# Kernel tuning notes

Measured on AMD Instinct MI355X. Metric: run time of the kernel, lower is better.

Reference implementation:

```python
import jax, jax.numpy as jnp
import numpy as np

VOCAB, EMB, QLEN, DLEN, K = 100000, 300, 256, 8192, 5


def prelu(x, a):
    return jnp.where(x >= 0, x, a * x)


def apply_conv(x, filt, a):
    # x: (L, E), filt: (E, 1, fs, E) -- matches torch F.conv2d(OIHW)
    fs = filt.shape[2]
    pad = fs // 2 + 1
    inp = x[None, None, :, :]  # (1,1,L,E)
    out = jax.lax.conv_general_dilated(
        inp, filt, window_strides=(1, 1), padding=[(pad, pad), (0, 0)],
        dimension_numbers=('NCHW', 'OIHW', 'NCHW'))  # (1,E,L',1)
    out = prelu(out, a)
    out = out[:, :, -x.shape[0]:, 0]          # keep last L rows -> (1,E,L)
    out = jnp.transpose(out, (0, 2, 1))[0]    # (L,E)
    return out + x


def cosine_sim(A, B):
    # (Q,E) x (D,E) -> (Q,D)
    num = A @ B.T
    den = jnp.linalg.norm(A, axis=1)[:, None] * jnp.linalg.norm(B, axis=1)[None, :]
    return num / den


def pool(sim):
    # sort-based k-max pooling == top_k (same set of values)
    top = jax.lax.top_k(sim, K)[0]           # (Q,K) descending
    avg = top.sum(-1) / float(K)
    mx = top[..., 0]
    return jnp.stack([mx, avg], axis=-1)      # (Q,2)


def score(pooled_list, w1, b1, w2, b2, a1, a2):
    x = jnp.concatenate(pooled_list, axis=-1)  # (Q,8)
    lo = prelu(x @ w1.T + b1, a1)              # dropout is identity in eval
    lo = prelu(lo @ w2.T + b2, a2)[..., 0]     # (Q,)
    return lo.sum(-1) / lo.shape[-1]


def setup_inputs() -> dict:
    key = jax.random.key(0)
    ks = jax.random.split(key, 12)
    doc1 = jax.random.randint(ks[0], (DLEN,), 0, VOCAB)
    doc2 = jax.random.randint(ks[1], (DLEN,), 0, VOCAB)
    question = jax.random.randint(ks[2], (QLEN,), 0, VOCAB)
    doc1_sim = jax.random.uniform(ks[3], (DLEN, QLEN), dtype=jnp.float32)
    doc2_sim = jax.random.uniform(ks[4], (DLEN, QLEN), dtype=jnp.float32)
    embeds = jax.random.normal(ks[5], (VOCAB, EMB), dtype=jnp.float32)
    filt_bi = jax.random.normal(ks[6], (EMB, 1, 2, EMB), dtype=jnp.float32)
    filt_tri = jax.random.normal(ks[7], (EMB, 1, 3, EMB), dtype=jnp.float32)
    w1 = jax.random.normal(ks[8], (8, 8), dtype=jnp.float32) * 0.3
    b1 = jnp.zeros((8,), jnp.float32)
    w2 = jax.random.normal(ks[9], (1, 8), dtype=jnp.float32) * 0.3
    b2 = jnp.zeros((1,), jnp.float32)
    a_bi = jnp.float32(0.25); a_tri = jnp.float32(0.25)
    a1 = jnp.float32(0.25); a2 = jnp.float32(0.25)
    return dict(doc1=doc1, doc2=doc2, question=question, doc1_sim=doc1_sim,
                doc2_sim=doc2_sim, embeds=embeds, filt_bi=filt_bi,
                filt_tri=filt_tri, a_bi=a_bi, a_tri=a_tri, w1=w1, b1=b1,
                w2=w2, b2=b2, a1=a1, a2=a2)


def reference(doc1, doc2, question, doc1_sim, doc2_sim, embeds, filt_bi,
              filt_tri, a_bi, a_tri, w1, b1, w2, b2, a1, a2):
    sim_oh1 = doc1_sim.T  # (Q,D)
    sim_oh2 = doc2_sim.T
    qe = embeds[question]
    d1e = embeds[doc1]
    d2e = embeds[doc2]
    qmask = (question > 1).astype(jnp.float32)
    m1 = qmask[:, None] * (doc1 > 1).astype(jnp.float32)[None, :]
    m2 = qmask[:, None] * (doc2 > 1).astype(jnp.float32)[None, :]
    ins1 = cosine_sim(qe, d1e) * m1
    ins2 = cosine_sim(qe, d2e) * m2
    q_bi = apply_conv(qe, filt_bi, a_bi)
    q_tri = apply_conv(qe, filt_tri, a_tri)
    d1_bi = apply_conv(d1e, filt_bi, a_bi)
    d1_tri = apply_conv(d1e, filt_tri, a_tri)
    d2_bi = apply_conv(d2e, filt_bi, a_bi)
    d2_tri = apply_conv(d2e, filt_tri, a_tri)
    s1_bi = cosine_sim(q_bi, d1_bi)
    s2_bi = cosine_sim(q_bi, d2_bi)
    s1_tri = cosine_sim(q_tri, d1_tri)
    s2_tri = cosine_sim(q_tri, d2_tri)
    d1_emit = score([pool(sim_oh1), pool(ins1), pool(s1_bi), pool(s1_tri)],
                    w1, b1, w2, b2, a1, a2)
    d2_emit = score([pool(sim_oh2), pool(ins2), pool(s2_bi), pool(s2_tri)],
                    w1, b1, w2, b2, a1, a2)
    # MarginRankingLoss(margin=0.9), y=1, batch of 1
    loss1 = jnp.maximum(0.0, -(d1_emit - d2_emit) + 0.9)
    loss2 = loss1 * 0.0
    return (loss1, d1_emit, d2_emit, loss1, loss2)
```

## Files before the change

### kernel.cpp

```cpp
#include <hip/hip_runtime.h>

#define EMB   300
#define QLEN  256
#define DLEN  8192
#define KTOP  5
#define STR   320
#define STRB  640

typedef __attribute__((ext_vector_type(8))) short short8v;
typedef __attribute__((ext_vector_type(4))) float f32x4;

__device__ inline float bf2f(short u) {
    return __uint_as_float(((unsigned int)(unsigned short)u) << 16);
}
__device__ inline short f2bf(float f) {
    unsigned int x = __float_as_uint(f);
    unsigned int r = x + 0x7fffu + ((x >> 16) & 1u);
    return (short)(r >> 16);
}
__device__ inline void gload_lds16(const void* g, void* l) {
    __builtin_amdgcn_global_load_lds((const __attribute__((address_space(1))) void*)g,
                                     (__attribute__((address_space(3))) void*)l, 16, 0, 0);
}
__device__ inline int swz128(int a) { return a ^ (((a >> 7) & 7) << 4); }

#define INSERT5(arr, v)                                                          \
    if ((v) > arr[4]) {                                                          \
        arr[4] = (v);                                                            \
        if (arr[4] > arr[3]) { float t_ = arr[4]; arr[4] = arr[3]; arr[3] = t_; }\
        if (arr[3] > arr[2]) { float t_ = arr[3]; arr[3] = arr[2]; arr[2] = t_; }\
        if (arr[2] > arr[1]) { float t_ = arr[2]; arr[2] = arr[1]; arr[1] = t_; }\
        if (arr[1] > arr[0]) { float t_ = arr[1]; arr[1] = arr[0]; arr[0] = t_; }\
    }

struct PrepArgs {
    const float* embeds;
    const int* toks[3]; short* out[3]; float* ssq[3]; int rows[3];
    const float* filt[2]; short* fout[2];
};

__global__ void prep(PrepArgs pa) {
    int W = blockIdx.x * 4 + (threadIdx.x >> 6);
    int lane = threadIdx.x & 63;
    int e0 = lane * 8;
    if (W < 16664) {
        int s, r;
        if (W < 264) { s = 0; r = W; }
        else if (W < 8464) { s = 1; r = W - 264; }
        else { s = 2; r = W - 8464; }
        int rows = pa.rows[s];
        short8v ov = {0, 0, 0, 0, 0, 0, 0, 0};
        float sum = 0.f;
        if (r < rows && e0 < 300) {
            const float* src = pa.embeds + (long)pa.toks[s][r] * EMB;
            float4 f0 = *(const float4*)(src + e0);
            ov[0] = f2bf(f0.x); ov[1] = f2bf(f0.y); ov[2] = f2bf(f0.z); ov[3] = f2bf(f0.w);
            sum = f0.x * f0.x + f0.y * f0.y + f0.z * f0.z + f0.w * f0.w;
            if (e0 < 296) {
                float4 f1 = *(const float4*)(src + e0 + 4);
                ov[4] = f2bf(f1.x); ov[5] = f2bf(f1.y); ov[6] = f2bf(f1.z); ov[7] = f2bf(f1.w);
                sum += f1.x * f1.x + f1.y * f1.y + f1.z * f1.z + f1.w * f1.w;
            }
        }
        if (e0 < STR) *(short8v*)(pa.out[s] + (long)r * STR + e0) = ov;
        #pragma unroll
        for (int off = 32; off > 0; off >>= 1) sum += __shfl_down(sum, off, 64);
        if (lane == 0 && r < rows) pa.ssq[s][r] = sum;
    } else {
        int w2 = W - 16664;
        int s = (w2 < 768) ? 0 : 1;
        int R = (s == 0) ? w2 : w2 - 768;
        int o = (s == 0) ? (R >> 1) : (R / 3);
        short8v ov = {0, 0, 0, 0, 0, 0, 0, 0};
        if (o < EMB && e0 < 300) {
            const float* src = pa.filt[s] + (long)R * EMB;
            float4 f0 = *(const float4*)(src + e0);
            ov[0] = f2bf(f0.x); ov[1] = f2bf(f0.y); ov[2] = f2bf(f0.z); ov[3] = f2bf(f0.w);
            if (e0 < 296) {
                float4 f1 = *(const float4*)(src + e0 + 4);
                ov[4] = f2bf(f1.x); ov[5] = f2bf(f1.y); ov[6] = f2bf(f1.z); ov[7] = f2bf(f1.w);
            }
        }
        if (e0 < STR) *(short8v*)(pa.fout[s] + (long)R * STR + e0) = ov;
    }
}

#define GEMM_PRELUDE64                                                        \
    int tid = threadIdx.x, lane = tid & 63, w = tid >> 6;                     \
    int wr = w >> 1, wc = w & 1;                                              \
    int arow[2], acol[2], brow[4], bcol[4];                                   \
    _Pragma("unroll")                                                         \
    for (int i_ = 0; i_ < 2; ++i_) {                                          \
        int lg_ = swz128(w * 2048 + i_ * 1024 + lane * 16);                   \
        arow[i_] = lg_ >> 7; acol[i_] = lg_ & 127;                            \
    }                                                                         \
    _Pragma("unroll")                                                         \
    for (int i_ = 0; i_ < 4; ++i_) {                                          \
        int lg_ = swz128(w * 4096 + i_ * 1024 + lane * 16);                   \
        brow[i_] = lg_ >> 7; bcol[i_] = lg_ & 127;                            \
    }

#define STAGE64(t) do { int kb_ = (t) * 128;                                  \
    _Pragma("unroll")                                                         \
    for (int i_ = 0; i_ < 2; ++i_)                                            \
        gload_lds16(Ab + (size_t)arow[i_] * STRB + kb_ + acol[i_],            \
                    AsB + w * 2048 + i_ * 1024);                              \
    _Pragma("unroll")                                                         \
    for (int i_ = 0; i_ < 4; ++i_)                                            \
        gload_lds16(Bb + (size_t)brow[i_] * ldbB + kb_ + bcol[i_],            \
                    BsB + w * 4096 + i_ * 1024);                              \
    } while (0)

#define COMPUTE64 do {                                                        \
    _Pragma("unroll")                                                         \
    for (int h_ = 0; h_ < 2; ++h_) {                                          \
        short8v a_[2], b_[4];                                                 \
        _Pragma("unroll")                                                     \
        for (int f_ = 0; f_ < 2; ++f_) {                                      \
            int la_ = (wr * 32 + f_ * 16 + (lane & 15)) * 128                 \
                      + ((lane >> 4) << 4) + h_ * 64;                         \
            a_[f_] = *(const short8v*)(AsB + swz128(la_));                    \
        }                                                                     \
        _Pragma("unroll")                                                     \
        for (int f_ = 0; f_ < 4; ++f_) {                                      \
            int lb_ = (wc * 64 + f_ * 16 + (lane & 15)) * 128                 \
                      + ((lane >> 4) << 4) + h_ * 64;                         \
            b_[f_] = *(const short8v*)(BsB + swz128(lb_));                    \
        }                                                                     \
        _Pragma("unroll")                                                     \
        for (int mf_ = 0; mf_ < 2; ++mf_)                                     \
            _Pragma("unroll")                                                 \
            for (int nf_ = 0; nf_ < 4; ++nf_)                                 \
                acc[mf_][nf_] = __builtin_amdgcn_mfma_f32_16x16x32_bf16(      \
                    a_[mf_], b_[nf_], acc[mf_][nf_], 0, 0, 0);                \
    } } while (0)

#define GEMM_MAIN64(nt) do {                                                  \
    for (int t_ = 0; t_ < (nt); ++t_) {                                       \
        if (t_ > 0) __syncthreads();                                          \
        STAGE64(t_);                                                          \
        __syncthreads();                                                      \
        COMPUTE64;                                                            \
    } } while (0)

__device__ inline void topk_reduce_store(float top[KTOP], float (*buf)[KTOP], int t,
                                         float* feat, int q, int c0) {
    #pragma unroll
    for (int i = 0; i < KTOP; ++i) buf[t][i] = top[i];
    __syncthreads();
    for (int stride = 128; stride >= 1; stride >>= 1) {
        if (t < stride) {
            float arr[KTOP];
            #pragma unroll
            for (int i = 0; i < KTOP; ++i) arr[i] = buf[t][i];
            #pragma unroll
            for (int r = 0; r < KTOP; ++r) { float v = buf[t + stride][r]; INSERT5(arr, v); }
            #pragma unroll
            for (int i = 0; i < KTOP; ++i) buf[t][i] = arr[i];
        }
        __syncthreads();
    }
    if (t == 0) {
        float mx = buf[0][0];
        float sum = buf[0][0] + buf[0][1] + buf[0][2] + buf[0][3] + buf[0][4];
        feat[(long)q * 8 + c0] = mx;
        feat[(long)q * 8 + c0 + 1] = sum / (float)KTOP;
    }
}

struct ConvSlice { const short* A; const short* F; short* O; float* ssq;
                   const float* alpha; int fs; int shift; };
struct ConvOhArgs { ConvSlice s[6]; const float* S1; const float* S2; float* part; };

__global__ __launch_bounds__(256) void conv_oh(ConvOhArgs args) {
    int orig = blockIdx.x;
    if (orig < 256) {
        int doc = orig >> 7, dblk = orig & 127;
        const float* S = doc == 0 ? args.S1 : args.S2;
        int t = threadIdx.x;
        const float* base = S + (size_t)dblk * 64 * QLEN + t;
        float top[KTOP];
        #pragma unroll
        for (int i = 0; i < KTOP; ++i) top[i] = -3.4e38f;
        float vb[16];
        #pragma unroll
        for (int g = 0; g < 4; ++g) {
            #pragma unroll
            for (int j = 0; j < 16; ++j)
                vb[j] = base[(size_t)(g * 16 + j) * QLEN];
            #pragma unroll
            for (int j = 0; j < 16; ++j) INSERT5(top, vb[j]);
        }
        float* dst = args.part + ((size_t)((6 + doc) * 128 + dblk) * QLEN + t) * KTOP;
        #pragma unroll
        for (int i = 0; i < KTOP; ++i) dst[i] = top[i];
        return;
    }
    int lin = orig - 256;
    int o = (lin & 7) * 195 + (lin >> 3);
    int z;
    if (o < 12) { z = 0; }
    else if (o < 24) { z = 1; o -= 12; }
    else { o -= 24; z = 2 + o / 384; o -= (z - 2) * 384; }
    ConvSlice sl;
    switch (z) {
        case 0: sl = args.s[0]; break; case 1: sl = args.s[1]; break;
        case 2: sl = args.s[2]; break; case 3: sl = args.s[3]; break;
        case 4: sl = args.s[4]; break; default: sl = args.s[5]; break;
    }
    int x = o % 3, y = o / 3;
    int m0 = y * 64, n0 = x * 128;
    int ldbB = sl.fs * STRB;

    __shared__ char smem[24576];
    char* AsB = smem;
    char* BsB = smem + 8192;
    GEMM_PRELUDE64
    const char* Ab = (const char*)sl.A + (size_t)(m0 + sl.shift) * STRB;
    const char* Bb = (const char*)sl.F + (size_t)n0 * ldbB;
    int nt = sl.fs * 5;
    float al = *sl.alpha;

    f32x4 acc[2][4] = {};
    GEMM_MAIN64(nt);

    #pragma unroll
    for (int mf = 0; mf < 2; ++mf) {
        #pragma unroll
        for (int j = 0; j < 4; ++j) {
            int r = m0 + wr * 32 + mf * 16 + (lane >> 4) * 4 + j;
            float p = 0.f;
            #pragma unroll
            for (int nf = 0; nf < 4; ++nf) {
                int c = n0 + wc * 64 + nf * 16 + (lane & 15);
                short ov = 0;
                if (c < EMB) {
                    float v = acc[mf][nf][j];
                    v = v >= 0.f ? v : al * v;
                    v += bf2f(sl.A[(size_t)r * STR + c]);
                    ov = f2bf(v);
                    p += v * v;
                }
                if (c < STR) sl.O[(size_t)r * STR + c] = ov;
            }
            p += __shfl_xor(p, 1, 64);
            p += __shfl_xor(p, 2, 64);
            p += __shfl_xor(p, 4, 64);
            p += __shfl_xor(p, 8, 64);
            if ((lane & 15) == 0) atomicAdd(sl.ssq + r, p);
        }
    }
}

struct SimSlice { const short* D; const short* Q; const float* dssq; const float* qssq;
                  const int* dtok; int mask; };
struct SimArgs { SimSlice s[6]; const int* qtok; float* part; };

__global__ __launch_bounds__(256) void sim_mfma(SimArgs args) {
    int lin = blockIdx.x;
    int wk = (lin & 7) * 192 + (lin >> 3);
    int s = wk >> 8; int rem = wk & 255; int x = rem & 1; int dblk = rem >> 1;
    SimSlice sl;
    switch (s) {
        case 0: sl = args.s[0]; break; case 1: sl = args.s[1]; break;
        case 2: sl = args.s[2]; break; case 3: sl = args.s[3]; break;
        case 4: sl = args.s[4]; break; default: sl = args.s[5]; break;
    }
    int m0 = dblk * 64, n0 = x * 128;
    const int ldbB = STRB;

    __shared__ char AsB[8192];
    __shared__ char BsB[16384];
    GEMM_PRELUDE64
    const char* Ab = (const char*)sl.D + (size_t)m0 * STRB;
    const char* Bb = (const char*)sl.Q + (size_t)n0 * STRB;

    f32x4 acc[2][4] = {};
    GEMM_MAIN64(5);

    float dinvv[2][4];
    int dtokv[2][4];
    #pragma unroll
    for (int mf = 0; mf < 2; ++mf) {
        int r0 = m0 + wr * 32 + mf * 16 + (lane >> 4) * 4;
        float4 dv = *(const float4*)(sl.dssq + r0);
        dinvv[mf][0] = rsqrtf(dv.x); dinvv[mf][1] = rsqrtf(dv.y);
        dinvv[mf][2] = rsqrtf(dv.z); dinvv[mf][3] = rsqrtf(dv.w);
        if (sl.mask) {
            int4 tv = *(const int4*)(sl.dtok + r0);
            dtokv[mf][0] = tv.x; dtokv[mf][1] = tv.y; dtokv[mf][2] = tv.z; dtokv[mf][3] = tv.w;
        }
    }
    __syncthreads();
    float (*lds5)[128][KTOP] = (float (*)[128][KTOP])AsB;

    #pragma unroll
    for (int nf = 0; nf < 4; ++nf) {
        int c = n0 + wc * 64 + nf * 16 + (lane & 15);
        float qs = rsqrtf(sl.qssq[c]);
        bool qok = sl.mask ? (args.qtok[c] > 1) : true;
        float top[KTOP];
        #pragma unroll
        for (int i = 0; i < KTOP; ++i) top[i] = -3.4e38f;
        #pragma unroll
        for (int mf = 0; mf < 2; ++mf)
            #pragma unroll
            for (int j = 0; j < 4; ++j) {
                float v = acc[mf][nf][j] * qs * dinvv[mf][j];
                if (sl.mask && (!qok || dtokv[mf][j] <= 1)) v = 0.f;
                INSERT5(top, v);
            }
        #pragma unroll
        for (int st = 16; st <= 32; st <<= 1) {
            float o[KTOP];
            #pragma unroll
            for (int i = 0; i < KTOP; ++i) o[i] = __shfl_xor(top[i], st, 64);
            #pragma unroll
            for (int i = 0; i < KTOP; ++i) { float v = o[i]; INSERT5(top, v); }
        }
        if (lane < 16) {
            int ql = wc * 64 + nf * 16 + lane;
            #pragma unroll
            for (int i = 0; i < KTOP; ++i) lds5[wr][ql][i] = top[i];
        }
    }
    __syncthreads();
    if (tid < 128) {
        float arr[KTOP];
        #pragma unroll
        for (int i = 0; i < KTOP; ++i) arr[i] = lds5[0][tid][i];
        #pragma unroll
        for (int i = 0; i < KTOP; ++i) { float v = lds5[1][tid][i]; INSERT5(arr, v); }
        int q = n0 + tid;
        float* dst = args.part + ((size_t)(s * 128 + dblk) * QLEN + q) * KTOP;
        #pragma unroll
        for (int i = 0; i < KTOP; ++i) dst[i] = arr[i];
    }
}

__global__ void pool_reduce(const float* __restrict__ part,
                            float* __restrict__ feat1, float* __restrict__ feat2) {
    int s = blockIdx.y, q = blockIdx.x, t = threadIdx.x;
    __shared__ float buf[256][KTOP];
    float top[KTOP];
    #pragma unroll
    for (int i = 0; i < KTOP; ++i) top[i] = -3.4e38f;
    if (t < 128) {
        const float* src = part + ((size_t)(s * 128 + t) * QLEN + q) * KTOP;
        #pragma unroll
        for (int i = 0; i < KTOP; ++i) { float v = src[i]; INSERT5(top, v); }
    }
    float* feat = (s < 6) ? (s < 3 ? feat1 : feat2) : (s == 6 ? feat1 : feat2);
    int c0 = (s < 6) ? 2 + 2 * (s % 3) : 0;
    topk_reduce_store(top, buf, t, feat, q, c0);
}

__global__ void final_score(const float* __restrict__ feat1, const float* __restrict__ feat2,
                            const float* __restrict__ w1, const float* __restrict__ b1,
                            const float* __restrict__ w2, const float* __restrict__ b2,
                            const float* __restrict__ a1p, const float* __restrict__ a2p,
                            float* __restrict__ out) {
    __shared__ float s1buf[256], s2buf[256];
    int q = threadIdx.x;
    float a1 = *a1p, a2 = *a2p;
    float v[2];
    #pragma unroll
    for (int dsel = 0; dsel < 2; ++dsel) {
        const float* feat = dsel == 0 ? feat1 : feat2;
        float x[8];
        #pragma unroll
        for (int i = 0; i < 8; ++i) x[i] = feat[q * 8 + i];
        float lo[8];
        #pragma unroll
        for (int j = 0; j < 8; ++j) {
            float s = b1[j];
            #pragma unroll
            for (int i = 0; i < 8; ++i) s += x[i] * w1[j * 8 + i];
            lo[j] = s >= 0.f ? s : a1 * s;
        }
        float s2v = b2[0];
        #pragma unroll
        for (int j = 0; j < 8; ++j) s2v += lo[j] * w2[j];
        v[dsel] = s2v >= 0.f ? s2v : a2 * s2v;
    }
    s1buf[q] = v[0];
    s2buf[q] = v[1];
    __syncthreads();
    for (int st = 128; st >= 1; st >>= 1) {
        if (q < st) { s1buf[q] += s1buf[q + st]; s2buf[q] += s2buf[q + st]; }
        __syncthreads();
    }
    if (q == 0) {
        float d1 = s1buf[0] / (float)QLEN;
        float d2 = s2buf[0] / (float)QLEN;
        float loss1 = fmaxf(0.f, -(d1 - d2) + 0.9f);
        out[0] = loss1; out[1] = d1; out[2] = d2; out[3] = loss1; out[4] = 0.f;
    }
}

extern "C" void kernel_launch(void* const* d_in, const int* in_sizes, int n_in,
                              void* d_out, int out_size, void* d_ws, size_t ws_size,
                              hipStream_t stream) {
    const int*   doc1     = (const int*)d_in[0];
    const int*   doc2     = (const int*)d_in[1];
    const int*   question = (const int*)d_in[2];
    const float* doc1_sim = (const float*)d_in[3];
    const float* doc2_sim = (const float*)d_in[4];
    const float* embeds   = (const float*)d_in[5];
    const float* filt_bi  = (const float*)d_in[6];
    const float* filt_tri = (const float*)d_in[7];
    const float* a_bi     = (const float*)d_in[8];
    const float* a_tri    = (const float*)d_in[9];
    const float* w1       = (const float*)d_in[10];
    const float* b1       = (const float*)d_in[11];
    const float* w2       = (const float*)d_in[12];
    const float* b2       = (const float*)d_in[13];
    const float* a1       = (const float*)d_in[14];
    const float* a2       = (const float*)d_in[15];
    float* out = (float*)d_out;

    float* ws = (float*)d_ws;
    size_t off = 0;
    auto allocf = [&](size_t n) { float* p = ws + off; off += n; return p; };
    float* feat1 = allocf(QLEN * 8);
    float* feat2 = allocf(QLEN * 8);
    float* ssq_qe  = allocf(QLEN);
    float* ssq_d1e = allocf(DLEN);
    float* ssq_d2e = allocf(DLEN);
    float* convssq = allocf(2 * QLEN + 4 * DLEN);
    float* ssq_qbi  = convssq;
    float* ssq_qtri = convssq + QLEN;
    float* ssq_d1bi  = convssq + 2 * QLEN;
    float* ssq_d1tri = convssq + 2 * QLEN + DLEN;
    float* ssq_d2bi  = convssq + 2 * QLEN + 2 * DLEN;
    float* ssq_d2tri = convssq + 2 * QLEN + 3 * DLEN;
    float* part = allocf((size_t)8 * 128 * QLEN * KTOP);
    off = (off + 7) & ~(size_t)7;

    short* hb = (short*)(ws + off);
    size_t hoff = 0;
    auto alloch = [&](size_t n) { short* p = hb + hoff; hoff += n; return p; };
    const size_t QH = (size_t)(QLEN + 8) * STR;
    const size_t DH = (size_t)(DLEN + 8) * STR;
    short* qe_h   = alloch(QH);
    short* qbi_h  = alloch(QH);
    short* qtri_h = alloch(QH);
    short* d1e_h   = alloch(DH);
    short* d1bi_h  = alloch(DH);
    short* d1tri_h = alloch(DH);
    short* d2e_h   = alloch(DH);
    short* d2bi_h  = alloch(DH);
    short* d2tri_h = alloch(DH);
    short* fbi_h  = alloch((size_t)384 * 2 * STR);
    short* ftri_h = alloch((size_t)384 * 3 * STR);

    hipMemsetAsync(convssq, 0, (2 * QLEN + 4 * DLEN) * sizeof(float), stream);

    PrepArgs pa;
    pa.embeds = embeds;
    pa.toks[0] = question; pa.out[0] = qe_h;  pa.ssq[0] = ssq_qe;  pa.rows[0] = QLEN;
    pa.toks[1] = doc1;     pa.out[1] = d1e_h; pa.ssq[1] = ssq_d1e; pa.rows[1] = DLEN;
    pa.toks[2] = doc2;     pa.out[2] = d2e_h; pa.ssq[2] = ssq_d2e; pa.rows[2] = DLEN;
    pa.filt[0] = filt_bi;  pa.fout[0] = fbi_h;
    pa.filt[1] = filt_tri; pa.fout[1] = ftri_h;
    prep<<<dim3(4646), 256, 0, stream>>>(pa);

    ConvOhArgs ca;
    ca.s[0] = { qe_h,  fbi_h,  qbi_h,  ssq_qbi,  a_bi,  2, 1 };
    ca.s[1] = { qe_h,  ftri_h, qtri_h, ssq_qtri, a_tri, 3, 0 };
    ca.s[2] = { d1e_h, fbi_h,  d1bi_h, ssq_d1bi, a_bi,  2, 1 };
    ca.s[3] = { d1e_h, ftri_h, d1tri_h,ssq_d1tri,a_tri, 3, 0 };
    ca.s[4] = { d2e_h, fbi_h,  d2bi_h, ssq_d2bi, a_bi,  2, 1 };
    ca.s[5] = { d2e_h, ftri_h, d2tri_h,ssq_d2tri,a_tri, 3, 0 };
    ca.S1 = doc1_sim; ca.S2 = doc2_sim;
    ca.part = part;
    conv_oh<<<dim3(1816), 256, 0, stream>>>(ca);

    SimArgs sa;
    sa.s[0] = { d1e_h,   qe_h,   ssq_d1e,   ssq_qe,   doc1, 1 };
    sa.s[1] = { d1bi_h,  qbi_h,  ssq_d1bi,  ssq_qbi,  doc1, 0 };
    sa.s[2] = { d1tri_h, qtri_h, ssq_d1tri, ssq_qtri, doc1, 0 };
    sa.s[3] = { d2e_h,   qe_h,   ssq_d2e,   ssq_qe,   doc2, 1 };
    sa.s[4] = { d2bi_h,  qbi_h,  ssq_d2bi,  ssq_qbi,  doc2, 0 };
    sa.s[5] = { d2tri_h, qtri_h, ssq_d2tri, ssq_qtri, doc2, 0 };
    sa.qtok = question;
    sa.part = part;
    sim_mfma<<<dim3(1536), 256, 0, stream>>>(sa);

    pool_reduce<<<dim3(QLEN, 8), 256, 0, stream>>>(part, feat1, feat2);

    final_score<<<dim3(1), 256, 0, stream>>>(feat1, feat2, w1, b1, w2, b2, a1, a2, out);
}
```

Baseline: 111.5 us.

## Move embedding-similarity GEMMs into conv kernel and fold memset into prep

The two raw-embedding cosine-similarity slices, which depend only on prep output, now run as extra blocks inside the conv kernel rather than in the later sim kernel. This fills the conv launch's tail and shrinks the sim kernel from six slices to four. The hipMemsetAsync that zeroed the conv sum-of-squares buffer is replaced by extra blocks in the prep kernel, removing one launch. Each of the two kernels now carries more block-type branching, and the conv and embedding-sim blocks compete for the same compute units.

```diff
diff --git a/kernel.cpp b/kernel.cpp
--- a/kernel.cpp
+++ b/kernel.cpp
@@ -37,9 +37,18 @@
     const float* embeds;
     const int* toks[3]; short* out[3]; float* ssq[3]; int rows[3];
     const float* filt[2]; short* fout[2];
+    float* convssq;
 };
 
 __global__ void prep(PrepArgs pa) {
+    if (blockIdx.x >= 4646) {
+        int idx = (blockIdx.x - 4646) * 256 + threadIdx.x;
+        if (idx < 8320) {
+            float4 z = {0.f, 0.f, 0.f, 0.f};
+            *(float4*)(pa.convssq + idx * 4) = z;
+        }
+        return;
+    }
     int W = blockIdx.x * 4 + (threadIdx.x >> 6);
     int lane = threadIdx.x & 63;
     int e0 = lane * 8;
@@ -168,35 +177,121 @@
     }
 }
 
+struct SimSlice { const short* D; const short* Q; const float* dssq; const float* qssq;
+                  const int* dtok; int mask; };
+
+__device__ void sim_body(SimSlice sl, int x, int dblk, int sslot,
+                         const int* qtok, float* part, char* AsB, char* BsB) {
+    int m0 = dblk * 64, n0 = x * 128;
+    const int ldbB = STRB;
+    GEMM_PRELUDE64
+    const char* Ab = (const char*)sl.D + (size_t)m0 * STRB;
+    const char* Bb = (const char*)sl.Q + (size_t)n0 * STRB;
+
+    f32x4 acc[2][4] = {};
+    GEMM_MAIN64(5);
+
+    float dinvv[2][4];
+    int dtokv[2][4];
+    #pragma unroll
+    for (int mf = 0; mf < 2; ++mf) {
+        int r0 = m0 + wr * 32 + mf * 16 + (lane >> 4) * 4;
+        float4 dv = *(const float4*)(sl.dssq + r0);
+        dinvv[mf][0] = rsqrtf(dv.x); dinvv[mf][1] = rsqrtf(dv.y);
+        dinvv[mf][2] = rsqrtf(dv.z); dinvv[mf][3] = rsqrtf(dv.w);
+        if (sl.mask) {
+            int4 tv = *(const int4*)(sl.dtok + r0);
+            dtokv[mf][0] = tv.x; dtokv[mf][1] = tv.y; dtokv[mf][2] = tv.z; dtokv[mf][3] = tv.w;
+        }
+    }
+    __syncthreads();
+    float (*lds5)[128][KTOP] = (float (*)[128][KTOP])AsB;
+
+    #pragma unroll
+    for (int nf = 0; nf < 4; ++nf) {
+        int c = n0 + wc * 64 + nf * 16 + (lane & 15);
+        float qs = rsqrtf(sl.qssq[c]);
+        bool qok = sl.mask ? (qtok[c] > 1) : true;
+        float top[KTOP];
+        #pragma unroll
+        for (int i = 0; i < KTOP; ++i) top[i] = -3.4e38f;
+        #pragma unroll
+        for (int mf = 0; mf < 2; ++mf)
+            #pragma unroll
+            for (int j = 0; j < 4; ++j) {
+                float v = acc[mf][nf][j] * qs * dinvv[mf][j];
+                if (sl.mask && (!qok || dtokv[mf][j] <= 1)) v = 0.f;
+                INSERT5(top, v);
+            }
+        #pragma unroll
+        for (int st = 16; st <= 32; st <<= 1) {
+            float o[KTOP];
+            #pragma unroll
+            for (int i = 0; i < KTOP; ++i) o[i] = __shfl_xor(top[i], st, 64);
+            #pragma unroll
+            for (int i = 0; i < KTOP; ++i) { float v = o[i]; INSERT5(top, v); }
+        }
+        if (lane < 16) {
+            int ql = wc * 64 + nf * 16 + lane;
+            #pragma unroll
+            for (int i = 0; i < KTOP; ++i) lds5[wr][ql][i] = top[i];
+        }
+    }
+    __syncthreads();
+    if (tid < 128) {
+        float arr[KTOP];
+        #pragma unroll
+        for (int i = 0; i < KTOP; ++i) arr[i] = lds5[0][tid][i];
+        #pragma unroll
+        for (int i = 0; i < KTOP; ++i) { float v = lds5[1][tid][i]; INSERT5(arr, v); }
+        int q = n0 + tid;
+        float* dst = part + ((size_t)(sslot * 128 + dblk) * QLEN + q) * KTOP;
+        #pragma unroll
+        for (int i = 0; i < KTOP; ++i) dst[i] = arr[i];
+    }
+}
+
 struct ConvSlice { const short* A; const short* F; short* O; float* ssq;
                    const float* alpha; int fs; int shift; };
-struct ConvOhArgs { ConvSlice s[6]; const float* S1; const float* S2; float* part; };
+struct ConvOhArgs { ConvSlice s[6]; const float* S1; const float* S2; float* part;
+                    SimSlice se[2]; const int* qtok; };
 
 __global__ __launch_bounds__(256) void conv_oh(ConvOhArgs args) {
+    __shared__ char smem[24576];
     int orig = blockIdx.x;
-    if (orig < 256) {
-        int doc = orig >> 7, dblk = orig & 127;
-        const float* S = doc == 0 ? args.S1 : args.S2;
-        int t = threadIdx.x;
-        const float* base = S + (size_t)dblk * 64 * QLEN + t;
-        float top[KTOP];
-        #pragma unroll
-        for (int i = 0; i < KTOP; ++i) top[i] = -3.4e38f;
-        float vb[16];
-        #pragma unroll
-        for (int g = 0; g < 4; ++g) {
-            #pragma unroll
-            for (int j = 0; j < 16; ++j)
-                vb[j] = base[(size_t)(g * 16 + j) * QLEN];
-            #pragma unroll
-            for (int j = 0; j < 16; ++j) INSERT5(top, vb[j]);
-        }
-        float* dst = args.part + ((size_t)((6 + doc) * 128 + dblk) * QLEN + t) * KTOP;
-        #pragma unroll
-        for (int i = 0; i < KTOP; ++i) dst[i] = top[i];
+    if (orig >= 1560) {
+        int r2 = orig - 1560;
+        if (r2 < 256) {
+            int doc = r2 >> 7, dblk = r2 & 127;
+            const float* S = doc == 0 ? args.S1 : args.S2;
+            int t = threadIdx.x;
+            const float* base = S + (size_t)dblk * 64 * QLEN + t;
+            float top[KTOP];
+            #pragma unroll
+            for (int i = 0; i < KTOP; ++i) top[i] = -3.4e38f;
+            float vb[16];
+            #pragma unroll
+            for (int g = 0; g < 4; ++g) {
+                #pragma unroll
+                for (int j = 0; j < 16; ++j)
+                    vb[j] = base[(size_t)(g * 16 + j) * QLEN];
+                #pragma unroll
+                for (int j = 0; j < 16; ++j) INSERT5(top, vb[j]);
+            }
+            float* dst = args.part + ((size_t)((6 + doc) * 128 + dblk) * QLEN + t) * KTOP;
+            #pragma unroll
+            for (int i = 0; i < KTOP; ++i) dst[i] = top[i];
+        } else {
+            int e = r2 - 256;
+            int which = e >> 8;
+            int rem = e & 255;
+            int x = rem & 1, dblk = rem >> 1;
+            sim_body(args.se[which], x, dblk, which == 0 ? 0 : 3,
+                     args.qtok, args.part, smem, smem + 8192);
+        }
         return;
     }
-    int lin = orig - 256;
+    int lin = orig;
     int o = (lin & 7) * 195 + (lin >> 3);
     int z;
     if (o < 12) { z = 0; }
@@ -212,7 +307,6 @@
     int m0 = y * 64, n0 = x * 128;
     int ldbB = sl.fs * STRB;
 
-    __shared__ char smem[24576];
     char* AsB = smem;
     char* BsB = smem + 8192;
     GEMM_PRELUDE64
@@ -252,90 +346,23 @@
     }
 }
 
-struct SimSlice { const short* D; const short* Q; const float* dssq; const float* qssq;
-                  const int* dtok; int mask; };
-struct SimArgs { SimSlice s[6]; const int* qtok; float* part; };
+struct SimArgs { SimSlice s[4]; int slot[4]; const int* qtok; float* part; };
 
 __global__ __launch_bounds__(256) void sim_mfma(SimArgs args) {
     int lin = blockIdx.x;
-    int wk = (lin & 7) * 192 + (lin >> 3);
-    int s = wk >> 8; int rem = wk & 255; int x = rem & 1; int dblk = rem >> 1;
+    int wk = (lin & 7) * 128 + (lin >> 3);
+    int si = wk >> 8; int rem = wk & 255; int x = rem & 1; int dblk = rem >> 1;
     SimSlice sl;
-    switch (s) {
-        case 0: sl = args.s[0]; break; case 1: sl = args.s[1]; break;
-        case 2: sl = args.s[2]; break; case 3: sl = args.s[3]; break;
-        case 4: sl = args.s[4]; break; default: sl = args.s[5]; break;
-    }
-    int m0 = dblk * 64, n0 = x * 128;
-    const int ldbB = STRB;
-
+    int sslot;
+    switch (si) {
+        case 0: sl = args.s[0]; sslot = args.slot[0]; break;
+        case 1: sl = args.s[1]; sslot = args.slot[1]; break;
+        case 2: sl = args.s[2]; sslot = args.slot[2]; break;
+        default: sl = args.s[3]; sslot = args.slot[3]; break;
+    }
     __shared__ char AsB[8192];
     __shared__ char BsB[16384];
-    GEMM_PRELUDE64
-    const char* Ab = (const char*)sl.D + (size_t)m0 * STRB;
-    const char* Bb = (const char*)sl.Q + (size_t)n0 * STRB;
-
-    f32x4 acc[2][4] = {};
-    GEMM_MAIN64(5);
-
-    float dinvv[2][4];
-    int dtokv[2][4];
-    #pragma unroll
-    for (int mf = 0; mf < 2; ++mf) {
-        int r0 = m0 + wr * 32 + mf * 16 + (lane >> 4) * 4;
-        float4 dv = *(const float4*)(sl.dssq + r0);
-        dinvv[mf][0] = rsqrtf(dv.x); dinvv[mf][1] = rsqrtf(dv.y);
-        dinvv[mf][2] = rsqrtf(dv.z); dinvv[mf][3] = rsqrtf(dv.w);
-        if (sl.mask) {
-            int4 tv = *(const int4*)(sl.dtok + r0);
-            dtokv[mf][0] = tv.x; dtokv[mf][1] = tv.y; dtokv[mf][2] = tv.z; dtokv[mf][3] = tv.w;
-        }
-    }
-    __syncthreads();
-    float (*lds5)[128][KTOP] = (float (*)[128][KTOP])AsB;
-
-    #pragma unroll
-    for (int nf = 0; nf < 4; ++nf) {
-        int c = n0 + wc * 64 + nf * 16 + (lane & 15);
-        float qs = rsqrtf(sl.qssq[c]);
-        bool qok = sl.mask ? (args.qtok[c] > 1) : true;
-        float top[KTOP];
-        #pragma unroll
-        for (int i = 0; i < KTOP; ++i) top[i] = -3.4e38f;
-        #pragma unroll
-        for (int mf = 0; mf < 2; ++mf)
-            #pragma unroll
-            for (int j = 0; j < 4; ++j) {
-                float v = acc[mf][nf][j] * qs * dinvv[mf][j];
-                if (sl.mask && (!qok || dtokv[mf][j] <= 1)) v = 0.f;
-                INSERT5(top, v);
-            }
-        #pragma unroll
-        for (int st = 16; st <= 32; st <<= 1) {
-            float o[KTOP];
-            #pragma unroll
-            for (int i = 0; i < KTOP; ++i) o[i] = __shfl_xor(top[i], st, 64);
-            #pragma unroll
-            for (int i = 0; i < KTOP; ++i) { float v = o[i]; INSERT5(top, v); }
-        }
-        if (lane < 16) {
-            int ql = wc * 64 + nf * 16 + lane;
-            #pragma unroll
-            for (int i = 0; i < KTOP; ++i) lds5[wr][ql][i] = top[i];
-        }
-    }
-    __syncthreads();
-    if (tid < 128) {
-        float arr[KTOP];
-        #pragma unroll
-        for (int i = 0; i < KTOP; ++i) arr[i] = lds5[0][tid][i];
-        #pragma unroll
-        for (int i = 0; i < KTOP; ++i) { float v = lds5[1][tid][i]; INSERT5(arr, v); }
-        int q = n0 + tid;
-        float* dst = args.part + ((size_t)(s * 128 + dblk) * QLEN + q) * KTOP;
-        #pragma unroll
-        for (int i = 0; i < KTOP; ++i) dst[i] = arr[i];
-    }
+    sim_body(sl, x, dblk, sslot, args.qtok, args.part, AsB, BsB);
 }
 
 __global__ void pool_reduce(const float* __restrict__ part,
@@ -454,8 +481,6 @@
     short* fbi_h  = alloch((size_t)384 * 2 * STR);
     short* ftri_h = alloch((size_t)384 * 3 * STR);
 
-    hipMemsetAsync(convssq, 0, (2 * QLEN + 4 * DLEN) * sizeof(float), stream);
-
     PrepArgs pa;
     pa.embeds = embeds;
     pa.toks[0] = question; pa.out[0] = qe_h;  pa.ssq[0] = ssq_qe;  pa.rows[0] = QLEN;
@@ -463,7 +488,8 @@
     pa.toks[2] = doc2;     pa.out[2] = d2e_h; pa.ssq[2] = ssq_d2e; pa.rows[2] = DLEN;
     pa.filt[0] = filt_bi;  pa.fout[0] = fbi_h;
     pa.filt[1] = filt_tri; pa.fout[1] = ftri_h;
-    prep<<<dim3(4646), 256, 0, stream>>>(pa);
+    pa.convssq = convssq;
+    prep<<<dim3(4679), 256, 0, stream>>>(pa);
 
     ConvOhArgs ca;
     ca.s[0] = { qe_h,  fbi_h,  qbi_h,  ssq_qbi,  a_bi,  2, 1 };
@@ -474,18 +500,19 @@
     ca.s[5] = { d2e_h, ftri_h, d2tri_h,ssq_d2tri,a_tri, 3, 0 };
     ca.S1 = doc1_sim; ca.S2 = doc2_sim;
     ca.part = part;
-    conv_oh<<<dim3(1816), 256, 0, stream>>>(ca);
+    ca.se[0] = { d1e_h, qe_h, ssq_d1e, ssq_qe, doc1, 1 };
+    ca.se[1] = { d2e_h, qe_h, ssq_d2e, ssq_qe, doc2, 1 };
+    ca.qtok = question;
+    conv_oh<<<dim3(2328), 256, 0, stream>>>(ca);
 
     SimArgs sa;
-    sa.s[0] = { d1e_h,   qe_h,   ssq_d1e,   ssq_qe,   doc1, 1 };
-    sa.s[1] = { d1bi_h,  qbi_h,  ssq_d1bi,  ssq_qbi,  doc1, 0 };
-    sa.s[2] = { d1tri_h, qtri_h, ssq_d1tri, ssq_qtri, doc1, 0 };
-    sa.s[3] = { d2e_h,   qe_h,   ssq_d2e,   ssq_qe,   doc2, 1 };
-    sa.s[4] = { d2bi_h,  qbi_h,  ssq_d2bi,  ssq_qbi,  doc2, 0 };
-    sa.s[5] = { d2tri_h, qtri_h, ssq_d2tri, ssq_qtri, doc2, 0 };
+    sa.s[0] = { d1bi_h,  qbi_h,  ssq_d1bi,  ssq_qbi,  doc1, 0 };  sa.slot[0] = 1;
+    sa.s[1] = { d1tri_h, qtri_h, ssq_d1tri, ssq_qtri, doc1, 0 };  sa.slot[1] = 2;
+    sa.s[2] = { d2bi_h,  qbi_h,  ssq_d2bi,  ssq_qbi,  doc2, 0 };  sa.slot[2] = 4;
+    sa.s[3] = { d2tri_h, qtri_h, ssq_d2tri, ssq_qtri, doc2, 0 };  sa.slot[3] = 5;
     sa.qtok = question;
     sa.part = part;
-    sim_mfma<<<dim3(1536), 256, 0, stream>>>(sa);
+    sim_mfma<<<dim3(1024), 256, 0, stream>>>(sa);
 
     pool_reduce<<<dim3(QLEN, 8), 256, 0, stream>>>(part, feat1, feat2);
 
```

Result: slower. 136.4 us (+22.3%).
